# Optimization experiments

Hardware: AMD Instinct MI355X
Metric: run time of the kernel (lower is better)

Reference implementation:

```python
import jax, jax.numpy as jnp
import numpy as np

N_NODES = 50000
N_EDGES = 800000
C_IN = 128
C_OUT = 128


def setup_inputs() -> dict:
    key = jax.random.key(0)
    k1, k2, k3, k4 = jax.random.split(key, 4)
    x = jax.random.normal(k1, (N_NODES, C_IN), dtype=jnp.float32)
    edge_index = jax.random.randint(k2, (2, N_EDGES), 0, N_NODES, dtype=jnp.int64)
    # Linear(in, out): weight [out, in], bias [out]
    W = jax.random.normal(k3, (C_OUT, C_IN), dtype=jnp.float32) * (1.0 / np.sqrt(C_IN))
    b = jax.random.normal(k4, (C_OUT,), dtype=jnp.float32) * 0.01
    return {"x": x, "edge_index": edge_index, "W": W, "b": b}


def reference(x, edge_index, W, b):
    # GCN layer: out = D^{-1/2} (A + I) D^{-1/2} x W^T + b
    # Implemented as sparse gather/segment-sum (same math as the dense
    # adjacency matmul in the original, without the O(N^2) blowup).
    n = x.shape[0]
    loops = jnp.arange(n, dtype=edge_index.dtype)
    row = jnp.concatenate([edge_index[0], loops])  # [E+N]
    col = jnp.concatenate([edge_index[1], loops])  # [E+N]
    # degree over col index (as in pyg_utils.degree(edge_index[1], ...))
    ones = jnp.ones(row.shape[0], dtype=x.dtype)
    deg = jax.ops.segment_sum(ones, col, num_segments=n)
    deg_inv_sqrt = jnp.where(deg > 0, jax.lax.rsqrt(deg), 0.0).astype(x.dtype)
    norm = deg_inv_sqrt[row] * deg_inv_sqrt[col]  # [E+N]
    # aggregate: out[i] = sum_{(i,j) in edges} norm * x[j]
    msgs = x[col] * norm[:, None]  # [E+N, C_in]
    agg = jax.ops.segment_sum(msgs, row, num_segments=n)  # [N, C_in]
    return agg @ W.T + b
```

## Files before the change

### kernel.cpp

```cpp
#include <hip/hip_runtime.h>
#include <hip/hip_bf16.h>
#include <hip/hip_fp16.h>

#define C 128
#define NCH 32768
#define CN 2
#define CNODES (CN * NCH)
#define BE 64

typedef _Float16 f16x8 __attribute__((ext_vector_type(8)));
typedef _Float16 f16x4 __attribute__((ext_vector_type(4)));
typedef float f32x4 __attribute__((ext_vector_type(4)));

__global__ __launch_bounds__(256) void k_hist(
        const int* __restrict__ row, const int* __restrict__ col,
        unsigned char* __restrict__ part_row, unsigned char* __restrict__ part_col,
        unsigned char* __restrict__ tag, int E,
        int* __restrict__ scol, int cap4, __half* __restrict__ Z16,
        unsigned* __restrict__ gbase, int n) {
    __shared__ unsigned lh[NCH / 4];
    int bid = blockIdx.x;
    int tid = threadIdx.x;
    if (bid >= 2 * CN * BE) {
        int fb = bid - 2 * CN * BE;
        int idx = fb * 256 + tid;
        if (idx < cap4) {
            int4 nv = make_int4(n, n, n, n);
            ((int4*)scol)[idx] = nv;
        }
        if (fb == 0) {
            if (tid < 16) {
                int pass = tid >> 3, g = tid & 7;
                ((uint4*)(Z16 + ((size_t)pass * (n + 1) + n) * 64))[g] =
                    make_uint4(0u, 0u, 0u, 0u);
            }
            if (tid == 16) *gbase = 0u;
        }
        return;
    }
    int side = (bid >= CN * BE) ? 1 : 0;
    int lb = side ? bid - CN * BE : bid;
    int c = lb >> 6;
    int b = lb & (BE - 1);
    for (int i = tid * 4; i < NCH / 4; i += 1024) {
        lh[i] = 0u; lh[i + 1] = 0u; lh[i + 2] = 0u; lh[i + 3] = 0u;
    }
    __syncthreads();
    int EPB = (E + BE - 1) / BE;
    int base = b * EPB;
    int end = min(base + EPB, E);
    const int* src = side ? col : row;

#define PROC_ROW(rv, ev)                                                  \
    if (((unsigned)(rv) >> 15) == (unsigned)c) {                          \
        int loc = (rv) & (NCH - 1);                                       \
        unsigned sh = ((unsigned)loc & 3u) << 3;                          \
        unsigned old = atomicAdd(&lh[loc >> 2], 1u << sh);                \
        tag[ev] = (unsigned char)((old >> sh) & 0xffu);                   \
    }
#define PROC_COL(rv)                                                      \
    if (((unsigned)(rv) >> 15) == (unsigned)c) {                          \
        int loc = (rv) & (NCH - 1);                                       \
        atomicAdd(&lh[loc >> 2], 1u << (((unsigned)loc & 3u) << 3));      \
    }
    int nv = 0;
    if ((((uintptr_t)(src + base)) & 15) == 0) nv = (end - base) >> 2;
    const int4* src4 = (const int4*)(src + base);
    if (!side) {
        for (int it = tid; it < nv; it += 256) {
            int4 v = src4[it];
            int e0 = base + it * 4;
            PROC_ROW(v.x, e0);
            PROC_ROW(v.y, e0 + 1);
            PROC_ROW(v.z, e0 + 2);
            PROC_ROW(v.w, e0 + 3);
        }
        for (int e = base + nv * 4 + tid; e < end; e += 256) {
            int r = src[e];
            PROC_ROW(r, e);
        }
    } else {
        for (int it = tid; it < nv; it += 256) {
            int4 v = src4[it];
            PROC_COL(v.x);
            PROC_COL(v.y);
            PROC_COL(v.z);
            PROC_COL(v.w);
        }
        for (int e = base + nv * 4 + tid; e < end; e += 256) {
            int r = src[e];
            PROC_COL(r);
        }
    }
#undef PROC_ROW
#undef PROC_COL
    __syncthreads();
    unsigned* dst = (unsigned*)((side ? part_col : part_row) + (size_t)b * CNODES + c * NCH);
    for (int i = tid; i < NCH / 4; i += 256) dst[i] = lh[i];
}

__global__ __launch_bounds__(256) void k_reduce_scan(
        unsigned char* __restrict__ part_row, const unsigned char* __restrict__ part_col,
        unsigned* __restrict__ start, unsigned* __restrict__ pcnt,
        unsigned* __restrict__ gbase, float* __restrict__ dis, int n) {
    __shared__ unsigned s[256];
    __shared__ unsigned base_sh;
    int t = threadIdx.x;
    int i = blockIdx.x * 256 + t;
    unsigned acc = 0;
    if (i < n) {
#pragma unroll 8
        for (int b = 0; b < BE; ++b) {
            size_t off = (size_t)b * CNODES + i;
            unsigned v = part_row[off];
            part_row[off] = (unsigned char)acc;
            acc += v;
        }
        unsigned d = 0;
#pragma unroll 8
        for (int b = 0; b < BE; ++b) d += part_col[(size_t)b * CNODES + i];
        dis[i] = rsqrtf((float)(d + 1u));
    }
    unsigned v = (i < n) ? ((acc + 15u) & ~15u) : 0u;
    s[t] = v;
    __syncthreads();
    for (int off = 1; off < 256; off <<= 1) {
        unsigned add = (t >= off) ? s[t - off] : 0u;
        __syncthreads();
        s[t] += add;
        __syncthreads();
    }
    if (t == 255) base_sh = atomicAdd(gbase, s[255]);
    __syncthreads();
    if (i < n) {
        start[i] = base_sh + s[t] - v;
        pcnt[i] = v;
    }
}

__global__ __launch_bounds__(256) void k_scatter_gemm(
        const int* __restrict__ row, const int* __restrict__ col,
        const unsigned char* __restrict__ tag, const unsigned char* __restrict__ boff,
        const unsigned* __restrict__ start, int* __restrict__ scol, int E, int SB,
        const float* __restrict__ A, const float* __restrict__ W,
        const float* __restrict__ dis, __half* __restrict__ Z16, int n) {
    __shared__ char lds[128 * 256];
    int bid = blockIdx.x;
    int tid = threadIdx.x;
    if (bid < SB) {
        int e = bid * 256 + tid;
        if (e < E) {
            int EPB = (E + BE - 1) / BE;
            unsigned b = (unsigned)e / (unsigned)EPB;
            int r = row[e];
            unsigned p = start[r] + boff[(size_t)b * CNODES + r] + tag[e];
            scol[p] = col[e];
        }
        return;
    }
    int w = tid >> 6, lane = tid & 63;
    int m0 = (bid - SB) * 128;

#pragma unroll
    for (int i = 0; i < 16; ++i) {
        int fidx = i * 256 + tid;
        int nr = fidx >> 5;
        int c4 = fidx & 31;
        float4 wv = *(const float4*)(W + (size_t)nr * C + c4 * 4);
        f16x4 hh = {(_Float16)wv.x, (_Float16)wv.y, (_Float16)wv.z, (_Float16)wv.w};
        unsigned byte = (unsigned)(nr * 256 + c4 * 8);
        byte ^= (unsigned)((nr & 7) << 4);
        *(f16x4*)(lds + byte) = hh;
    }
    __syncthreads();

    int rbase = m0 + w * 32;
    int q = lane >> 4, rl = lane & 15;
    float dm[2];
#pragma unroll
    for (int mt = 0; mt < 2; ++mt) {
        int r = rbase + mt * 16 + rl;
        dm[mt] = (r < n) ? dis[r] : 0.f;
    }
    f32x4 acc[2][8] = {};
#pragma unroll
    for (int kc = 0; kc < 4; ++kc) {
        f16x8 af[2];
#pragma unroll
        for (int mt = 0; mt < 2; ++mt) {
            int r = rbase + mt * 16 + rl;
            float4 x0 = make_float4(0.f, 0.f, 0.f, 0.f), x1 = x0;
            if (r < n) {
                const float* srcx = A + (size_t)r * C + kc * 32 + q * 8;
                x0 = *(const float4*)srcx;
                x1 = *(const float4*)(srcx + 4);
            }
            float s = dm[mt];
            af[mt][0] = (_Float16)(x0.x * s);
            af[mt][1] = (_Float16)(x0.y * s);
            af[mt][2] = (_Float16)(x0.z * s);
            af[mt][3] = (_Float16)(x0.w * s);
            af[mt][4] = (_Float16)(x1.x * s);
            af[mt][5] = (_Float16)(x1.y * s);
            af[mt][6] = (_Float16)(x1.z * s);
            af[mt][7] = (_Float16)(x1.w * s);
        }
#pragma unroll
        for (int nt = 0; nt < 8; ++nt) {
            int nrow = nt * 16 + rl;
            unsigned byte = (unsigned)(nrow * 256 + kc * 64 + q * 16);
            byte ^= (unsigned)((nrow & 7) << 4);
            f16x8 bf = *(f16x8*)(lds + byte);
            acc[0][nt] = __builtin_amdgcn_mfma_f32_16x16x32_f16(af[0], bf, acc[0][nt], 0, 0, 0);
            acc[1][nt] = __builtin_amdgcn_mfma_f32_16x16x32_f16(af[1], bf, acc[1][nt], 0, 0, 0);
        }
    }
    __syncthreads();

#pragma unroll
    for (int mt = 0; mt < 2; ++mt)
#pragma unroll
        for (int nt = 0; nt < 8; ++nt)
#pragma unroll
            for (int i = 0; i < 4; ++i) {
                int row_l = w * 32 + mt * 16 + q * 4 + i;
                int colh = nt * 16 + rl;
                unsigned byte = (unsigned)(row_l * 256 + colh * 2);
                byte ^= (unsigned)((row_l & 7) << 4);
                *(_Float16*)(lds + byte) = (_Float16)acc[mt][nt][i];
            }
    __syncthreads();

#pragma unroll
    for (int it = 0; it < 8; ++it) {
        int idx = it * 256 + tid;
        int row_l = idx >> 4, c8 = idx & 15;
        unsigned byte = (unsigned)(row_l * 256 + c8 * 16);
        byte ^= (unsigned)((row_l & 7) << 4);
        uint4 v = *(uint4*)(lds + byte);
        int gr = m0 + row_l;
        if (gr < n) {
            int pass = c8 >> 3;
            int g = c8 & 7;
            *(uint4*)(Z16 + ((size_t)pass * (n + 1) + gr) * 64 + g * 8) = v;
        }
    }
}

__device__ __forceinline__ void add8(uint4 v, float2& a0, float2& a1,
                                     float2& a2, float2& a3) {
    float2 f;
    f = __half22float2(*(__half2*)&v.x); a0.x += f.x; a0.y += f.y;
    f = __half22float2(*(__half2*)&v.y); a1.x += f.x; a1.y += f.y;
    f = __half22float2(*(__half2*)&v.z); a2.x += f.x; a2.y += f.y;
    f = __half22float2(*(__half2*)&v.w); a3.x += f.x; a3.y += f.y;
}

__global__ __launch_bounds__(256) void k_agg(const __half* __restrict__ Z16,
                                             const int* __restrict__ scol,
                                             const unsigned* __restrict__ start,
                                             const unsigned* __restrict__ pcnt,
                                             const float* __restrict__ dis,
                                             const float* __restrict__ bias,
                                             float* __restrict__ out, int n, int RPB) {
    int bid = blockIdx.x;
    int pass = (bid >= RPB) ? 1 : 0;
    int rb = bid - pass * RPB;
    int wid = threadIdx.x >> 6;
    int lane = threadIdx.x & 63;
    int rw = lane >> 5;
    int slot = (lane >> 3) & 3;
    int g = lane & 7;
    int r = rb * 8 + wid * 2 + rw;
    if (r >= n) return;
    unsigned s0 = start[r];
    unsigned s1 = s0 + pcnt[r];
    float dr = dis[r];
    const uint4* Z4 = (const uint4*)(Z16 + (size_t)pass * (n + 1) * 64);
    float2 a0 = {0.f, 0.f}, a1 = a0, a2 = a0, a3 = a0;
    if (slot == 0) {
        uint4 v = Z4[(size_t)r * 8 + g];
        add8(v, a0, a1, a2, a3);
    }
    for (unsigned k = s0; k < s1; k += 16) {
        int c0 = scol[k + slot];
        int c1 = scol[k + 4 + slot];
        int c2 = scol[k + 8 + slot];
        int c3 = scol[k + 12 + slot];
        uint4 v0 = Z4[(size_t)c0 * 8 + g];
        uint4 v1 = Z4[(size_t)c1 * 8 + g];
        uint4 v2 = Z4[(size_t)c2 * 8 + g];
        uint4 v3 = Z4[(size_t)c3 * 8 + g];
        add8(v0, a0, a1, a2, a3);
        add8(v1, a0, a1, a2, a3);
        add8(v2, a0, a1, a2, a3);
        add8(v3, a0, a1, a2, a3);
    }
    a0.x += __shfl_xor(a0.x, 8);  a0.y += __shfl_xor(a0.y, 8);
    a1.x += __shfl_xor(a1.x, 8);  a1.y += __shfl_xor(a1.y, 8);
    a2.x += __shfl_xor(a2.x, 8);  a2.y += __shfl_xor(a2.y, 8);
    a3.x += __shfl_xor(a3.x, 8);  a3.y += __shfl_xor(a3.y, 8);
    a0.x += __shfl_xor(a0.x, 16); a0.y += __shfl_xor(a0.y, 16);
    a1.x += __shfl_xor(a1.x, 16); a1.y += __shfl_xor(a1.y, 16);
    a2.x += __shfl_xor(a2.x, 16); a2.y += __shfl_xor(a2.y, 16);
    a3.x += __shfl_xor(a3.x, 16); a3.y += __shfl_xor(a3.y, 16);
    if (slot == 0) {
        const float* bp = bias + pass * 64 + g * 8;
        float4 b0 = *(const float4*)bp;
        float4 b1 = *(const float4*)(bp + 4);
        float4 o0, o1;
        o0.x = b0.x + dr * a0.x; o0.y = b0.y + dr * a0.y;
        o0.z = b0.z + dr * a1.x; o0.w = b0.w + dr * a1.y;
        o1.x = b1.x + dr * a2.x; o1.y = b1.y + dr * a2.y;
        o1.z = b1.z + dr * a3.x; o1.w = b1.w + dr * a3.y;
        float* op = out + (size_t)r * C + pass * 64 + g * 8;
        *(float4*)op = o0;
        *(float4*)(op + 4) = o1;
    }
}

extern "C" void kernel_launch(void* const* d_in, const int* in_sizes, int n_in,
                              void* d_out, int out_size, void* d_ws, size_t ws_size,
                              hipStream_t stream) {
    const float* x  = (const float*)d_in[0];
    const int*   ei = (const int*)d_in[1];
    const float* W  = (const float*)d_in[2];
    const float* b  = (const float*)d_in[3];
    float* out = (float*)d_out;

    int n = in_sizes[0] / C;
    int E = in_sizes[1] / 2;
    const int* row = ei;
    const int* col = ei + E;

    char* p = (char*)d_ws;
    size_t cap  = (size_t)E + 15 * (size_t)n;
    size_t sz_part = (((size_t)BE * CNODES) + 511) & ~(size_t)511;
    size_t sz_n    = (((size_t)n * 4) + 511) & ~(size_t)511;
    size_t sz_E1   = (((size_t)E) + 511) & ~(size_t)511;
    size_t sz_cap  = ((cap * 4) + 511) & ~(size_t)511;
    size_t off = 0;
    unsigned char*  part_row = (unsigned char*)(p + off);  off += sz_part;
    unsigned char*  part_col = (unsigned char*)(p + off);  off += sz_part;
    unsigned*       start    = (unsigned*)(p + off);       off += sz_n;
    unsigned*       pcnt     = (unsigned*)(p + off);       off += sz_n;
    float*          dis      = (float*)(p + off);          off += sz_n;
    unsigned*       gbase    = (unsigned*)(p + off);       off += 512;
    unsigned char*  tag      = (unsigned char*)(p + off);  off += sz_E1;
    int*            scol     = (int*)(p + off);            off += sz_cap;
    __half*         z16      = (__half*)(p + off);

    int NT = 256;
    int NB = (n + NT - 1) / NT;
    int SB = (E + NT - 1) / NT;
    int GB = (n + 127) / 128;
    int cap4 = (int)((cap + 3) / 4);
    int FB = (cap4 + NT - 1) / NT;
    int RPB = (n + 7) / 8;

    k_hist<<<2 * CN * BE + FB, NT, 0, stream>>>(row, col, part_row, part_col, tag, E,
                                                scol, cap4, z16, gbase, n);
    k_reduce_scan<<<NB, NT, 0, stream>>>(part_row, part_col, start, pcnt, gbase, dis, n);
    k_scatter_gemm<<<SB + GB, NT, 0, stream>>>(row, col, tag, part_row, start, scol,
                                               E, SB, x, W, dis, z16, n);
    k_agg<<<2 * RPB, NT, 0, stream>>>(z16, scol, start, pcnt, dis, b, out, n, RPB);
}
```

Measured before the change: 76.82 us.

## Fill only padding slots of scol in scan and halve GEMM row tile

```diff
diff --git a/kernel.cpp b/kernel.cpp
--- a/kernel.cpp
+++ b/kernel.cpp
@@ -16,26 +16,17 @@
         const int* __restrict__ row, const int* __restrict__ col,
         unsigned char* __restrict__ part_row, unsigned char* __restrict__ part_col,
         unsigned char* __restrict__ tag, int E,
-        int* __restrict__ scol, int cap4, __half* __restrict__ Z16,
-        unsigned* __restrict__ gbase, int n) {
+        __half* __restrict__ Z16, unsigned* __restrict__ gbase, int n) {
     __shared__ unsigned lh[NCH / 4];
     int bid = blockIdx.x;
     int tid = threadIdx.x;
     if (bid >= 2 * CN * BE) {
-        int fb = bid - 2 * CN * BE;
-        int idx = fb * 256 + tid;
-        if (idx < cap4) {
-            int4 nv = make_int4(n, n, n, n);
-            ((int4*)scol)[idx] = nv;
-        }
-        if (fb == 0) {
-            if (tid < 16) {
-                int pass = tid >> 3, g = tid & 7;
-                ((uint4*)(Z16 + ((size_t)pass * (n + 1) + n) * 64))[g] =
-                    make_uint4(0u, 0u, 0u, 0u);
-            }
-            if (tid == 16) *gbase = 0u;
-        }
+        if (tid < 16) {
+            int pass = tid >> 3, g = tid & 7;
+            ((uint4*)(Z16 + ((size_t)pass * (n + 1) + n) * 64))[g] =
+                make_uint4(0u, 0u, 0u, 0u);
+        }
+        if (tid == 16) *gbase = 0u;
         return;
     }
     int side = (bid >= CN * BE) ? 1 : 0;
@@ -102,7 +93,8 @@
 __global__ __launch_bounds__(256) void k_reduce_scan(
         unsigned char* __restrict__ part_row, const unsigned char* __restrict__ part_col,
         unsigned* __restrict__ start, unsigned* __restrict__ pcnt,
-        unsigned* __restrict__ gbase, float* __restrict__ dis, int n) {
+        unsigned* __restrict__ gbase, float* __restrict__ dis,
+        int* __restrict__ scol, int n) {
     __shared__ unsigned s[256];
     __shared__ unsigned base_sh;
     int t = threadIdx.x;
@@ -133,8 +125,10 @@
     if (t == 255) base_sh = atomicAdd(gbase, s[255]);
     __syncthreads();
     if (i < n) {
-        start[i] = base_sh + s[t] - v;
+        unsigned sb = base_sh + s[t] - v;
+        start[i] = sb;
         pcnt[i] = v;
+        for (unsigned k = acc; k < v; ++k) scol[sb + k] = n;
     }
 }
 
@@ -159,7 +153,7 @@
         return;
     }
     int w = tid >> 6, lane = tid & 63;
-    int m0 = (bid - SB) * 128;
+    int m0 = (bid - SB) * 64;
 
 #pragma unroll
     for (int i = 0; i < 16; ++i) {
@@ -174,65 +168,52 @@
     }
     __syncthreads();
 
-    int rbase = m0 + w * 32;
     int q = lane >> 4, rl = lane & 15;
-    float dm[2];
-#pragma unroll
-    for (int mt = 0; mt < 2; ++mt) {
-        int r = rbase + mt * 16 + rl;
-        dm[mt] = (r < n) ? dis[r] : 0.f;
-    }
-    f32x4 acc[2][8] = {};
+    int r = m0 + w * 16 + rl;
+    float dm = (r < n) ? dis[r] : 0.f;
+    f32x4 acc[8] = {};
 #pragma unroll
     for (int kc = 0; kc < 4; ++kc) {
-        f16x8 af[2];
-#pragma unroll
-        for (int mt = 0; mt < 2; ++mt) {
-            int r = rbase + mt * 16 + rl;
-            float4 x0 = make_float4(0.f, 0.f, 0.f, 0.f), x1 = x0;
-            if (r < n) {
-                const float* srcx = A + (size_t)r * C + kc * 32 + q * 8;
-                x0 = *(const float4*)srcx;
-                x1 = *(const float4*)(srcx + 4);
-            }
-            float s = dm[mt];
-            af[mt][0] = (_Float16)(x0.x * s);
-            af[mt][1] = (_Float16)(x0.y * s);
-            af[mt][2] = (_Float16)(x0.z * s);
-            af[mt][3] = (_Float16)(x0.w * s);
-            af[mt][4] = (_Float16)(x1.x * s);
-            af[mt][5] = (_Float16)(x1.y * s);
-            af[mt][6] = (_Float16)(x1.z * s);
-            af[mt][7] = (_Float16)(x1.w * s);
-        }
+        f16x8 af;
+        float4 x0 = make_float4(0.f, 0.f, 0.f, 0.f), x1 = x0;
+        if (r < n) {
+            const float* srcx = A + (size_t)r * C + kc * 32 + q * 8;
+            x0 = *(const float4*)srcx;
+            x1 = *(const float4*)(srcx + 4);
+        }
+        af[0] = (_Float16)(x0.x * dm);
+        af[1] = (_Float16)(x0.y * dm);
+        af[2] = (_Float16)(x0.z * dm);
+        af[3] = (_Float16)(x0.w * dm);
+        af[4] = (_Float16)(x1.x * dm);
+        af[5] = (_Float16)(x1.y * dm);
+        af[6] = (_Float16)(x1.z * dm);
+        af[7] = (_Float16)(x1.w * dm);
 #pragma unroll
         for (int nt = 0; nt < 8; ++nt) {
             int nrow = nt * 16 + rl;
             unsigned byte = (unsigned)(nrow * 256 + kc * 64 + q * 16);
             byte ^= (unsigned)((nrow & 7) << 4);
             f16x8 bf = *(f16x8*)(lds + byte);
-            acc[0][nt] = __builtin_amdgcn_mfma_f32_16x16x32_f16(af[0], bf, acc[0][nt], 0, 0, 0);
-            acc[1][nt] = __builtin_amdgcn_mfma_f32_16x16x32_f16(af[1], bf, acc[1][nt], 0, 0, 0);
-        }
-    }
-    __syncthreads();
-
-#pragma unroll
-    for (int mt = 0; mt < 2; ++mt)
-#pragma unroll
-        for (int nt = 0; nt < 8; ++nt)
-#pragma unroll
-            for (int i = 0; i < 4; ++i) {
-                int row_l = w * 32 + mt * 16 + q * 4 + i;
-                int colh = nt * 16 + rl;
-                unsigned byte = (unsigned)(row_l * 256 + colh * 2);
-                byte ^= (unsigned)((row_l & 7) << 4);
-                *(_Float16*)(lds + byte) = (_Float16)acc[mt][nt][i];
-            }
-    __syncthreads();
-
-#pragma unroll
-    for (int it = 0; it < 8; ++it) {
+            acc[nt] = __builtin_amdgcn_mfma_f32_16x16x32_f16(af, bf, acc[nt], 0, 0, 0);
+        }
+    }
+    __syncthreads();
+
+#pragma unroll
+    for (int nt = 0; nt < 8; ++nt)
+#pragma unroll
+        for (int i = 0; i < 4; ++i) {
+            int row_l = w * 16 + q * 4 + i;
+            int colh = nt * 16 + rl;
+            unsigned byte = (unsigned)(row_l * 256 + colh * 2);
+            byte ^= (unsigned)((row_l & 7) << 4);
+            *(_Float16*)(lds + byte) = (_Float16)acc[nt][i];
+        }
+    __syncthreads();
+
+#pragma unroll
+    for (int it = 0; it < 4; ++it) {
         int idx = it * 256 + tid;
         int row_l = idx >> 4, c8 = idx & 15;
         unsigned byte = (unsigned)(row_l * 256 + c8 * 16);
@@ -353,14 +334,13 @@
     int NT = 256;
     int NB = (n + NT - 1) / NT;
     int SB = (E + NT - 1) / NT;
-    int GB = (n + 127) / 128;
-    int cap4 = (int)((cap + 3) / 4);
-    int FB = (cap4 + NT - 1) / NT;
+    int GB = (n + 63) / 64;
     int RPB = (n + 7) / 8;
 
-    k_hist<<<2 * CN * BE + FB, NT, 0, stream>>>(row, col, part_row, part_col, tag, E,
-                                                scol, cap4, z16, gbase, n);
-    k_reduce_scan<<<NB, NT, 0, stream>>>(part_row, part_col, start, pcnt, gbase, dis, n);
+    k_hist<<<2 * CN * BE + 1, NT, 0, stream>>>(row, col, part_row, part_col, tag, E,
+                                               z16, gbase, n);
+    k_reduce_scan<<<NB, NT, 0, stream>>>(part_row, part_col, start, pcnt, gbase, dis,
+                                         scol, n);
     k_scatter_gemm<<<SB + GB, NT, 0, stream>>>(row, col, tag, part_row, start, scol,
                                                E, SB, x, W, dis, z16, n);
     k_agg<<<2 * RPB, NT, 0, stream>>>(z16, scol, start, pcnt, dis, b, out, n, RPB);
```

Measured after the change: 77.15 us. Within noise of the previous version (+0.4%).
